# Kernel tuning notes

Hardware: AMD Instinct MI355X
Metric: run time of the kernel (lower is better)

## Reference

```python
import jax, jax.numpy as jnp
import numpy as np
import math

B = 128          # batch size
DS = 1024        # dim_s
DT = 1024        # dim_t
D = 128          # input_size (embed dim)
K = 16           # number of negatives
N = 100000       # output_size (memory bank rows)
T = 0.07         # NCE temperature
MOM = 0.5        # memory momentum


def _linear(x, W, b):
    # torch nn.Linear: y = x @ W.T + b, W is [out, in]
    return jnp.matmul(x, W.T) + b


def _l2norm(x, axis):
    # Normalize(power=2): x / (sum x^2)^(1/2)
    return x / jnp.sqrt(jnp.sum(x * x, axis=axis, keepdims=True))


def setup_inputs() -> dict:
    key = jax.random.key(0)
    ks = jax.random.split(key, 24)

    def lin_params(k1, k2, din, dout, scale=0.02):
        W = jax.random.normal(k1, (dout, din), dtype=jnp.float32) * scale
        b = jax.random.normal(k2, (dout,), dtype=jnp.float32) * scale
        return W, b

    inp = {}
    inp['s'] = jax.random.normal(ks[0], (B, DS), dtype=jnp.float32)
    inp['t'] = jax.random.normal(ks[1], (B, DT), dtype=jnp.float32)
    inp['y'] = jax.random.randint(ks[2], (B,), 0, N)
    inp['idx'] = jax.random.randint(ks[3], (B, B, K + 1), 0, N)

    stdv = 1.0 / math.sqrt(D / 3.0)
    inp['memory_s'] = jax.random.uniform(ks[4], (N, D), dtype=jnp.float32, minval=-stdv, maxval=stdv)

    inp['W_es'], inp['b_es'] = lin_params(ks[5], ks[6], DS, D)
    inp['W_et'], inp['b_et'] = lin_params(ks[7], ks[8], DT, D)
    inp['W_tv'], inp['b_tv'] = lin_params(ks[9], ks[10], D, D)
    inp['W_tq'], inp['b_tq'] = lin_params(ks[11], ks[12], D, D)
    inp['W_tsv'], inp['b_tsv'] = lin_params(ks[13], ks[14], D, D)
    inp['W_tsq'], inp['b_tsq'] = lin_params(ks[15], ks[16], D, D)
    inp['W_mt'], inp['b_mt'] = lin_params(ks[17], ks[18], D, D)
    inp['W_mts'], inp['b_mts'] = lin_params(ks[19], ks[20], D, D)
    inp['W_ht'], inp['b_ht'] = lin_params(ks[21], ks[22], D, D)
    inp['W_hts'], inp['b_hts'] = lin_params(ks[23], ks[22], D, D)
    return inp


def reference(s, t, y, idx, memory_s,
              W_es, b_es, W_et, b_et, W_tv, b_tv, W_tq, b_tq,
              W_tsv, b_tsv, W_tsq, b_tsq, W_mt, b_mt, W_mts, b_mts,
              W_ht, b_ht, W_hts, b_hts):
    idx_k = idx.reshape(B, B, -1)[:, :, :K]
    # gather negatives from memory bank (detached in the original)
    neg_s = jax.lax.stop_gradient(
        jnp.take(memory_s, idx_k.reshape(-1), axis=0).reshape(B, B, K, D))

    se = _linear(s, W_es, b_es)          # [B, D]
    te = _linear(t, W_et, b_et)          # [B, D]

    m_t_v = _linear(te, W_tv, b_tv)
    m_t_q = _linear(te, W_tq, b_tq)
    m_t_s_v = _linear(te, W_tsv, b_tsv)
    m_t_s_q_pos = _linear(se, W_tsq, b_tsq)
    m_t_s_q_neg = _linear(neg_s, W_tsq, b_tsq)   # [B, B, K, D]

    # broadcasted relation tensors: r[i, j] = relu(v[j] - q[i])
    r_t = _linear(jax.nn.relu(m_t_v[None, :, :] - m_t_q[:, None, :]), W_mt, b_mt)            # [B, B, D]
    r_t_s_pos = _linear(jax.nn.relu(m_t_s_v[None, :, :] - m_t_s_q_pos[:, None, :]), W_mts, b_mts)  # [B, B, D]
    r_t_s_neg = _linear(jax.nn.relu(m_t_s_v[None, :, None, :] - m_t_s_q_neg), W_mts, b_mts)  # [B, B, K, D]

    h_t = _l2norm(_linear(r_t, W_ht, b_ht), -1)                 # [B, B, D]
    h_t_s_pos = _l2norm(_linear(r_t_s_pos, W_hts, b_hts), -1)   # [B, B, D]
    h_t_s_neg = _l2norm(_linear(r_t_s_neg, W_hts, b_hts), -1)   # [B, B, K, D]
    h_t_s = jnp.concatenate([h_t_s_pos[:, :, None, :], h_t_s_neg], axis=2)  # [B, B, K+1, D]

    # momentum scatter update of the memory bank (no_grad in original)
    ab = jnp.take(memory_s, y, axis=0) * MOM + jax.lax.stop_gradient(se) * (1.0 - MOM)
    updated = ab / jnp.sqrt(jnp.sum(ab * ab, axis=1, keepdims=True))
    memory_new = memory_s.at[y].set(updated)

    scores = jnp.sum(h_t[:, :, None, :] * h_t_s, axis=3, keepdims=True)  # [B, B, K+1, 1]
    out = jnp.exp(scores / T) / jnp.exp(1.0 / T)
    return out.reshape(B * B, K + 1, 1), memory_new
```

## Files before the change

### kernel.cpp

```cpp
#include <hip/hip_runtime.h>


#define BB   128
#define DD   128
#define KK   16
#define NMEM 100000

static constexpr float INV_T = 1.0f / 0.07f;

#define WS_SE    0
#define WS_TE    16384
#define WS_MTV   32768
#define WS_MTQ   49152
#define WS_MSV   65536
#define WS_MSPQ  81920
#define WS_HT    98304
#define FR_TS_HI 2195456
#define FR_TS_LO 2203648
#define FR_T_HI  2211840
#define FR_T_LO  2220032
#define BC_TS    2244608
#define BC_T     2244736
#define WS_PROJ  2244864
#define OUT_MEM  278528

typedef __attribute__((ext_vector_type(8))) short short8v;
typedef __attribute__((ext_vector_type(4))) float f32x4;

__device__ inline void split2(float x0, float x1, unsigned& hi, unsigned& lo) {
    unsigned u0 = __float_as_uint(x0), u1 = __float_as_uint(x1);
    unsigned h0 = (u0 + 0x8000u) & 0xffff0000u;
    unsigned h1 = (u1 + 0x8000u) & 0xffff0000u;
    float l0 = x0 - __uint_as_float(h0);
    float l1 = x1 - __uint_as_float(h1);
    unsigned v0 = __float_as_uint(l0) + 0x8000u;
    unsigned v1 = __float_as_uint(l1) + 0x8000u;
    hi = __builtin_amdgcn_perm(h1, h0, 0x07060302u);
    lo = __builtin_amdgcn_perm(v1, v0, 0x07060302u);
}

__device__ inline void split8(const float4& x0, const float4& x1, short8v& h8, short8v& l8) {
    uint4 H, L;
    split2(x0.x, x0.y, H.x, L.x);
    split2(x0.z, x0.w, H.y, L.y);
    split2(x1.x, x1.y, H.z, L.z);
    split2(x1.z, x1.w, H.w, L.w);
    h8 = *(short8v*)&H;
    l8 = *(short8v*)&L;
}

__device__ inline void splits(float x, unsigned short& h, unsigned short& l) {
    unsigned u = __float_as_uint(x);
    unsigned hu = (u + 0x8000u) & 0xffff0000u;
    float lf = x - __uint_as_float(hu);
    h = (unsigned short)(hu >> 16);
    l = (unsigned short)((__float_as_uint(lf) + 0x8000u) >> 16);
}

__global__ __launch_bounds__(512, 2) void k_pre1b(
    const float* __restrict__ s, const float* __restrict__ t,
    const float* __restrict__ W_es, const float* __restrict__ b_es,
    const float* __restrict__ W_et, const float* __restrict__ b_et,
    const float* __restrict__ W_mts, const float* __restrict__ b_mts,
    const float* __restrict__ W_hts, const float* __restrict__ b_hts,
    const float* __restrict__ W_mt,  const float* __restrict__ b_mt,
    const float* __restrict__ W_ht,  const float* __restrict__ b_ht,
    float* __restrict__ ws)
{
    __shared__ float red[8][2048];
    int bid = blockIdx.x, tid = threadIdx.x;

    if (bid >= 16) {
        int cb = bid - 16;
        int which = cb >> 5;
        int sub = cb & 31;
        const float* A  = which ? W_ht : W_hts;
        const float* Bm = which ? W_mt : W_mts;
        short* FH = (short*)(ws + (which ? FR_T_HI : FR_TS_HI));
        short* FL = (short*)(ws + (which ? FR_T_LO : FR_TS_LO));

        int d = sub * 4 + (tid >> 7);
        int k = tid & 127;
        const float* Ar = A + d * 128;
        float acc = 0.f;
        #pragma unroll 8
        for (int m = 0; m < 128; ++m)
            acc = fmaf(Ar[m], Bm[m * 128 + k], acc);

        int t2 = d >> 4, col = d & 15, c = k >> 5, kg = (k >> 3) & 3, e = k & 7;
        int a2 = (((t2 * 4 + c) * 4 + kg) * 16 + col) * 8 + e;
        unsigned short h, l; splits(acc, h, l);
        FH[a2] = (short)h;
        FL[a2] = (short)l;

        if (sub == 0 && tid < 128) {
            const float* bin  = which ? b_mt : b_mts;
            const float* bout = which ? b_ht : b_hts;
            float a = bout[tid];
            #pragma unroll 8
            for (int m = 0; m < 128; ++m) a = fmaf(A[tid * 128 + m], bin[m], a);
            ws[(which ? BC_T : BC_TS) + tid] = a;
        }
        return;
    }

    int which = bid >> 3;
    int grp = bid & 7;
    const float* x    = which ? t : s;
    const float* W    = which ? W_et : W_es;
    const float* bias = which ? b_et : b_es;

    int lane = tid & 63, w = tid >> 6;
    int col = lane & 15, rq = lane >> 4;
    const float* xr = x + (long)(grp * 16 + col) * 1024;

    f32x4 acc[8];
    #pragma unroll
    for (int t2 = 0; t2 < 8; ++t2) {
        acc[t2][0] = 0.f; acc[t2][1] = 0.f; acc[t2][2] = 0.f; acc[t2][3] = 0.f;
    }

    #pragma unroll
    for (int c = 0; c < 4; ++c) {
        int kb = w * 128 + c * 32 + rq * 8;
        short8v ah, al;
        {
            float4 x0 = *(const float4*)&xr[kb];
            float4 x1 = *(const float4*)&xr[kb + 4];
            split8(x0, x1, ah, al);
        }
        #pragma unroll
        for (int t2 = 0; t2 < 8; ++t2) {
            const float* wr = W + (long)(t2 * 16 + col) * 1024 + kb;
            float4 w0 = *(const float4*)&wr[0];
            float4 w1 = *(const float4*)&wr[4];
            short8v bh, bl; split8(w0, w1, bh, bl);
            acc[t2] = __builtin_amdgcn_mfma_f32_16x16x32_bf16(al, bh, acc[t2], 0, 0, 0);
            acc[t2] = __builtin_amdgcn_mfma_f32_16x16x32_bf16(ah, bl, acc[t2], 0, 0, 0);
            acc[t2] = __builtin_amdgcn_mfma_f32_16x16x32_bf16(ah, bh, acc[t2], 0, 0, 0);
        }
    }

    #pragma unroll
    for (int t2 = 0; t2 < 8; ++t2)
        #pragma unroll
        for (int r = 0; r < 4; ++r)
            red[w][(rq * 4 + r) * 128 + t2 * 16 + col] = acc[t2][r];
    __syncthreads();

    for (int i = tid; i < 2048; i += 512) {
        float sum = 0.f;
        #pragma unroll
        for (int w2 = 0; w2 < 8; ++w2) sum += red[w2][i];
        int rl = i >> 7, d = i & 127;
        ws[(which ? WS_TE : WS_SE) + (grp * 16 + rl) * 128 + d] = sum + bias[d];
    }
}

__global__ __launch_bounds__(512, 2) void k_proj4(
    const float* __restrict__ W_tv,  const float* __restrict__ b_tv,
    const float* __restrict__ W_tq,  const float* __restrict__ b_tq,
    const float* __restrict__ W_tsv, const float* __restrict__ b_tsv,
    const float* __restrict__ W_tsq, const float* __restrict__ b_tsq,
    float* __restrict__ ws)
{
    int pb = blockIdx.x;
    int tid = threadIdx.x;
    int gi = tid >> 7, d = tid & 127;
    int rr = pb * 4 + gi;
    int which = rr >> 7, r = rr & 127;
    const float *W, *bias, *in;
    float* outp;
    switch (which) {
        case 0:  W = W_tv;  bias = b_tv;  in = ws + WS_TE; outp = ws + WS_MTV;  break;
        case 1:  W = W_tq;  bias = b_tq;  in = ws + WS_TE; outp = ws + WS_MTQ;  break;
        case 2:  W = W_tsv; bias = b_tsv; in = ws + WS_TE; outp = ws + WS_MSV;  break;
        default: W = W_tsq; bias = b_tsq; in = ws + WS_SE; outp = ws + WS_MSPQ; break;
    }
    const float* xr = in + r * DD;
    const float* Wr = W + d * DD;
    float a0 = 0.f, a1 = 0.f, a2 = 0.f, a3 = 0.f;
    #pragma unroll
    for (int k = 0; k < DD; k += 16) {
        float4 xv0 = *(const float4*)&xr[k],      wv0 = *(const float4*)&Wr[k];
        float4 xv1 = *(const float4*)&xr[k + 4],  wv1 = *(const float4*)&Wr[k + 4];
        float4 xv2 = *(const float4*)&xr[k + 8],  wv2 = *(const float4*)&Wr[k + 8];
        float4 xv3 = *(const float4*)&xr[k + 12], wv3 = *(const float4*)&Wr[k + 12];
        a0 = fmaf(xv0.x, wv0.x, fmaf(xv0.y, wv0.y, fmaf(xv0.z, wv0.z, fmaf(xv0.w, wv0.w, a0))));
        a1 = fmaf(xv1.x, wv1.x, fmaf(xv1.y, wv1.y, fmaf(xv1.z, wv1.z, fmaf(xv1.w, wv1.w, a1))));
        a2 = fmaf(xv2.x, wv2.x, fmaf(xv2.y, wv2.y, fmaf(xv2.z, wv2.z, fmaf(xv2.w, wv2.w, a2))));
        a3 = fmaf(xv3.x, wv3.x, fmaf(xv3.y, wv3.y, fmaf(xv3.z, wv3.z, fmaf(xv3.w, wv3.w, a3))));
    }
    outp[r * DD + d] = bias[d] + ((a0 + a1) + (a2 + a3));
}

__global__ __launch_bounds__(512, 2) void k_pre2c(
    const float* __restrict__ mem, const float* __restrict__ b_tsq,
    const float* __restrict__ W_tsq,
    float* __restrict__ ws, float* __restrict__ proj)
{
    __shared__ short Bh[16384], Bl[16384];
    int bid = blockIdx.x, tid = threadIdx.x;

    if (bid < 782) {
        {
            int d = tid >> 2, k0 = (tid & 3) * 32;
            int tt = d >> 4, col = d & 15;
            #pragma unroll
            for (int h = 0; h < 4; ++h) {
                int k = k0 + h * 8;
                float4 x0 = *(const float4*)&W_tsq[d * 128 + k];
                float4 x1 = *(const float4*)&W_tsq[d * 128 + k + 4];
                short8v h8, l8; split8(x0, x1, h8, l8);
                int c = k >> 5, kg = (k >> 3) & 3;
                int a2 = (((tt * 4 + c) * 4 + kg) * 16 + col) * 8;
                *(short8v*)&Bh[a2] = h8;
                *(short8v*)&Bl[a2] = l8;
            }
        }
        __syncthreads();

        int lane = tid & 63, w = tid >> 6;
        int g = bid * 8 + w;
        if (g >= 6250) return;

        int col = lane & 15, rq = lane >> 4;
        long rowA = (long)g * 16 + col;
        int kg = rq * 8;
        const float* src = mem + rowA * 128;

        short8v ah[4], al[4];
        #pragma unroll
        for (int c = 0; c < 4; ++c) {
            int ko = c * 32 + kg;
            float4 x0 = *(const float4*)&src[ko];
            float4 x1 = *(const float4*)&src[ko + 4];
            split8(x0, x1, ah[c], al[c]);
        }

        #pragma unroll
        for (int t = 0; t < 8; ++t) {
            float b0 = b_tsq[t * 16 + col];
            f32x4 a; a[0] = b0; a[1] = b0; a[2] = b0; a[3] = b0;
            #pragma unroll
            for (int c = 0; c < 4; ++c) {
                int off = ((t * 4 + c) * 64 + lane) * 8;
                short8v bh = *(const short8v*)&Bh[off];
                short8v bl = *(const short8v*)&Bl[off];
                a = __builtin_amdgcn_mfma_f32_16x16x32_bf16(al[c], bh, a, 0, 0, 0);
                a = __builtin_amdgcn_mfma_f32_16x16x32_bf16(ah[c], bl, a, 0, 0, 0);
                a = __builtin_amdgcn_mfma_f32_16x16x32_bf16(ah[c], bh, a, 0, 0, 0);
            }
            #pragma unroll
            for (int r = 0; r < 4; ++r)
                proj[((long)g * 16 + rq * 4 + r) * 128 + t * 16 + col] = a[r];
        }
        return;
    }

    {
        const short* frh = (const short*)(ws + FR_T_HI);
        const short* frl = (const short*)(ws + FR_T_LO);
        for (int i2 = tid; i2 < 2048; i2 += 512) {
            ((uint4*)Bh)[i2] = ((const uint4*)frh)[i2];
            ((uint4*)Bl)[i2] = ((const uint4*)frl)[i2];
        }
        __syncthreads();

        const float* mtv = ws + WS_MTV;
        const float* mtq = ws + WS_MTQ;
        const float* bc  = ws + BC_T;
        float* ht = ws + WS_HT;

        int lane = tid & 63, w = tid >> 6;
        int col = lane & 15, rq = lane >> 4;
        int g = (bid - 782) * 8 + w;
        int p = g * 16 + col;
        int i = p >> 7, j = p & 127;
        int kg = rq * 8;
        const float* vj = mtv + j * 128;
        const float* qi = mtq + i * 128;

        short8v ah[4], al[4];
        #pragma unroll
        for (int c = 0; c < 4; ++c) {
            int ko = c * 32 + kg;
            float4 v0 = *(const float4*)&vj[ko], v1 = *(const float4*)&vj[ko + 4];
            float4 q0 = *(const float4*)&qi[ko], q1 = *(const float4*)&qi[ko + 4];
            float4 r0 = make_float4(fmaxf(v0.x - q0.x, 0.f), fmaxf(v0.y - q0.y, 0.f),
                                    fmaxf(v0.z - q0.z, 0.f), fmaxf(v0.w - q0.w, 0.f));
            float4 r1 = make_float4(fmaxf(v1.x - q1.x, 0.f), fmaxf(v1.y - q1.y, 0.f),
                                    fmaxf(v1.z - q1.z, 0.f), fmaxf(v1.w - q1.w, 0.f));
            split8(r0, r1, ah[c], al[c]);
        }

        f32x4 acc[8];
        #pragma unroll
        for (int t = 0; t < 8; ++t) {
            float b0 = bc[t * 16 + col];
            f32x4 a; a[0] = b0; a[1] = b0; a[2] = b0; a[3] = b0;
            #pragma unroll
            for (int c = 0; c < 4; ++c) {
                int off = ((t * 4 + c) * 64 + lane) * 8;
                short8v bh = *(const short8v*)&Bh[off];
                short8v bl = *(const short8v*)&Bl[off];
                a = __builtin_amdgcn_mfma_f32_16x16x32_bf16(al[c], bh, a, 0, 0, 0);
                a = __builtin_amdgcn_mfma_f32_16x16x32_bf16(ah[c], bl, a, 0, 0, 0);
                a = __builtin_amdgcn_mfma_f32_16x16x32_bf16(ah[c], bh, a, 0, 0, 0);
            }
            acc[t] = a;
        }

        #pragma unroll
        for (int r = 0; r < 4; ++r) {
            long rho = g * 16 + rq * 4 + r;
            float s_uu = 0.f;
            #pragma unroll
            for (int t = 0; t < 8; ++t) { float u = acc[t][r]; s_uu = fmaf(u, u, s_uu); }
            #pragma unroll
            for (int m = 1; m < 16; m <<= 1) s_uu += __shfl_xor(s_uu, m);
            float rn = rsqrtf(s_uu);
            #pragma unroll
            for (int t = 0; t < 8; ++t)
                ht[rho * 128 + t * 16 + col] = acc[t][r] * rn;
        }
    }
}

__global__ __launch_bounds__(1024, 8) void k_neg_mfma(
    const float* __restrict__ ws, const int* __restrict__ idx,
    const float* __restrict__ proj, float* __restrict__ out,
    const float* __restrict__ mem, float* __restrict__ dst)
{
    int tid = threadIdx.x;
    if (blockIdx.x >= 1088) {
        long n4 = (long)NMEM * 128 / 4;
        long i = (long)(blockIdx.x - 1088) * 1024 + tid;
        for (; i < n4; i += 128 * 1024)
            ((float4*)dst)[i] = ((const float4*)mem)[i];
        return;
    }

    __shared__ short Bh[16384], Bl[16384];
    const short* frh = (const short*)(ws + FR_TS_HI);
    const short* frl = (const short*)(ws + FR_TS_LO);
    for (int i2 = tid; i2 < 2048; i2 += 1024) {
        ((uint4*)Bh)[i2] = ((const uint4*)frh)[i2];
        ((uint4*)Bl)[i2] = ((const uint4*)frl)[i2];
    }
    __syncthreads();

    const float* msv  = ws + WS_MSV;
    const float* mspq = ws + WS_MSPQ;
    const float* ht   = ws + WS_HT;
    const float* bc   = ws + BC_TS;

    int lane = tid & 63, w = tid >> 6;
    int col = lane & 15, rq = lane >> 4;
    int bswz = (blockIdx.x & 7) * 136 + (blockIdx.x >> 3);
    int g = bswz * 16 + w;

    int rowA = g * 16 + col;
    int p = rowA / 17;
    int slot = rowA - p * 17;
    const float* src = slot ? (proj + (long)idx[p * 17 + slot - 1] * 128)
                            : (mspq + (p >> 7) * 128);
    const float* vj = msv + (p & 127) * 128;
    int kg = rq * 8;

    short8v ah[4], al[4];
    #pragma unroll
    for (int c = 0; c < 4; ++c) {
        int ko = c * 32 + kg;
        float4 v0 = *(const float4*)&vj[ko],  v1 = *(const float4*)&vj[ko + 4];
        float4 q0 = *(const float4*)&src[ko], q1 = *(const float4*)&src[ko + 4];
        float4 r0 = make_float4(fmaxf(v0.x - q0.x, 0.f), fmaxf(v0.y - q0.y, 0.f),
                                fmaxf(v0.z - q0.z, 0.f), fmaxf(v0.w - q0.w, 0.f));
        float4 r1 = make_float4(fmaxf(v1.x - q1.x, 0.f), fmaxf(v1.y - q1.y, 0.f),
                                fmaxf(v1.z - q1.z, 0.f), fmaxf(v1.w - q1.w, 0.f));
        split8(r0, r1, ah[c], al[c]);
    }

    f32x4 acc[8];
    #pragma unroll
    for (int t = 0; t < 8; ++t) {
        float b0 = bc[t * 16 + col];
        f32x4 a; a[0] = b0; a[1] = b0; a[2] = b0; a[3] = b0;
        #pragma unroll
        for (int c = 0; c < 4; ++c) {
            int off = ((t * 4 + c) * 64 + lane) * 8;
            short8v bh = *(const short8v*)&Bh[off];
            short8v bl = *(const short8v*)&Bl[off];
            a = __builtin_amdgcn_mfma_f32_16x16x32_bf16(al[c], bh, a, 0, 0, 0);
            a = __builtin_amdgcn_mfma_f32_16x16x32_bf16(ah[c], bl, a, 0, 0, 0);
            a = __builtin_amdgcn_mfma_f32_16x16x32_bf16(ah[c], bh, a, 0, 0, 0);
        }
        acc[t] = a;
    }

    #pragma unroll
    for (int r = 0; r < 4; ++r) {
        int rho = g * 16 + rq * 4 + r;
        int pe = rho / 17;
        const float* hrow = ht + (long)pe * 128 + col;
        float s_uu = 0.f, s_hu = 0.f;
        #pragma unroll
        for (int t = 0; t < 8; ++t) {
            float u = acc[t][r];
            s_uu = fmaf(u, u, s_uu);
            s_hu = fmaf(hrow[t * 16], u, s_hu);
        }
        #pragma unroll
        for (int m = 1; m < 16; m <<= 1) {
            s_uu += __shfl_xor(s_uu, m);
            s_hu += __shfl_xor(s_hu, m);
        }
        if (col == 0)
            out[rho] = __expf((s_hu * rsqrtf(s_uu) - 1.0f) * INV_T);
    }
}

__global__ __launch_bounds__(128) void k_memupd(
    const float* __restrict__ mem, const float* __restrict__ se,
    const int* __restrict__ y, float* __restrict__ dst)
{
    int b = blockIdx.x;
    int d = threadIdx.x;
    int yb = y[b];
    for (int b2 = b + 1; b2 < BB; ++b2)
        if (y[b2] == yb) return;

    float ab = 0.5f * mem[(long)yb * 128 + d] + 0.5f * se[b * 128 + d];
    float ss = ab * ab;
    #pragma unroll
    for (int mq = 32; mq; mq >>= 1) ss += __shfl_xor(ss, mq);
    __shared__ float partial[2];
    if ((d & 63) == 0) partial[d >> 6] = ss;
    __syncthreads();
    float tot = partial[0] + partial[1];
    dst[(long)yb * 128 + d] = ab * rsqrtf(tot);
}

extern "C" void kernel_launch(void* const* d_in, const int* in_sizes, int n_in,
                              void* d_out, int out_size, void* d_ws, size_t ws_size,
                              hipStream_t stream)
{
    const float* s     = (const float*)d_in[0];
    const float* t     = (const float*)d_in[1];
    const int*   y     = (const int*)  d_in[2];
    const int*   idx   = (const int*)  d_in[3];
    const float* mem   = (const float*)d_in[4];
    const float* W_es  = (const float*)d_in[5];  const float* b_es  = (const float*)d_in[6];
    const float* W_et  = (const float*)d_in[7];  const float* b_et  = (const float*)d_in[8];
    const float* W_tv  = (const float*)d_in[9];  const float* b_tv  = (const float*)d_in[10];
    const float* W_tq  = (const float*)d_in[11]; const float* b_tq  = (const float*)d_in[12];
    const float* W_tsv = (const float*)d_in[13]; const float* b_tsv = (const float*)d_in[14];
    const float* W_tsq = (const float*)d_in[15]; const float* b_tsq = (const float*)d_in[16];
    const float* W_mt  = (const float*)d_in[17]; const float* b_mt  = (const float*)d_in[18];
    const float* W_mts = (const float*)d_in[19]; const float* b_mts = (const float*)d_in[20];
    const float* W_ht  = (const float*)d_in[21]; const float* b_ht  = (const float*)d_in[22];
    const float* W_hts = (const float*)d_in[23]; const float* b_hts = (const float*)d_in[24];

    float* out  = (float*)d_out;
    float* ws   = (float*)d_ws;
    float* proj = ws + WS_PROJ;

    k_pre1b   <<<80, 512, 0, stream>>>(s, t, W_es, b_es, W_et, b_et,
                                       W_mts, b_mts, W_hts, b_hts,
                                       W_mt, b_mt, W_ht, b_ht, ws);
    k_proj4   <<<128, 512, 0, stream>>>(W_tv, b_tv, W_tq, b_tq, W_tsv, b_tsv,
                                        W_tsq, b_tsq, ws);
    k_pre2c   <<<910, 512, 0, stream>>>(mem, b_tsq, W_tsq, ws, proj);
    k_neg_mfma<<<1216, 1024, 0, stream>>>(ws, idx, proj, out, mem, out + OUT_MEM);
    k_memupd  <<<128, 128, 0, stream>>>(mem, ws + WS_SE, y, out + OUT_MEM);
}
```

Before: 118.8 us.

## Move memory-bank projection into first kernel to overlap with encoder GEMMs

The memory-bank projection (mem @ W_tsq, 782 blocks) is moved out of the later pre2c kernel and into the first kernel, alongside the encoder linears and the weight-fold blocks. The h_t computation becomes its own small kernel. The bank projection depends only on inputs, so it can run concurrently with the small, latency-bound encoder work instead of queuing behind k_proj4. In exchange, the first kernel carries a uniform 64KB of shared memory for every block, and the small h_t kernel now runs alone after k_proj4.

```diff
diff --git a/kernel.cpp b/kernel.cpp
--- a/kernel.cpp
+++ b/kernel.cpp
@@ -57,7 +57,9 @@
     l = (unsigned short)((__float_as_uint(lf) + 0x8000u) >> 16);
 }
 
-__global__ __launch_bounds__(512, 2) void k_pre1b(
+__global__ __launch_bounds__(512, 2) void k_stage1(
+    const float* __restrict__ mem, const float* __restrict__ b_tsq,
+    const float* __restrict__ W_tsq,
     const float* __restrict__ s, const float* __restrict__ t,
     const float* __restrict__ W_es, const float* __restrict__ b_es,
     const float* __restrict__ W_et, const float* __restrict__ b_et,
@@ -65,13 +67,128 @@
     const float* __restrict__ W_hts, const float* __restrict__ b_hts,
     const float* __restrict__ W_mt,  const float* __restrict__ b_mt,
     const float* __restrict__ W_ht,  const float* __restrict__ b_ht,
-    float* __restrict__ ws)
-{
-    __shared__ float red[8][2048];
+    float* __restrict__ ws, float* __restrict__ proj)
+{
+    __shared__ __align__(16) char smem[65536];
+    short* Bh = (short*)smem;
+    short* Bl = (short*)(smem + 32768);
     int bid = blockIdx.x, tid = threadIdx.x;
 
-    if (bid >= 16) {
-        int cb = bid - 16;
+    if (bid < 782) {
+        {
+            int d = tid >> 2, k0 = (tid & 3) * 32;
+            int tt = d >> 4, col = d & 15;
+            #pragma unroll
+            for (int h = 0; h < 4; ++h) {
+                int k = k0 + h * 8;
+                float4 x0 = *(const float4*)&W_tsq[d * 128 + k];
+                float4 x1 = *(const float4*)&W_tsq[d * 128 + k + 4];
+                short8v h8, l8; split8(x0, x1, h8, l8);
+                int c = k >> 5, kg = (k >> 3) & 3;
+                int a2 = (((tt * 4 + c) * 4 + kg) * 16 + col) * 8;
+                *(short8v*)&Bh[a2] = h8;
+                *(short8v*)&Bl[a2] = l8;
+            }
+        }
+        __syncthreads();
+
+        int lane = tid & 63, w = tid >> 6;
+        int g = bid * 8 + w;
+        if (g >= 6250) return;
+
+        int col = lane & 15, rq = lane >> 4;
+        long rowA = (long)g * 16 + col;
+        int kg = rq * 8;
+        const float* src = mem + rowA * 128;
+
+        short8v ah[4], al[4];
+        #pragma unroll
+        for (int c = 0; c < 4; ++c) {
+            int ko = c * 32 + kg;
+            float4 x0 = *(const float4*)&src[ko];
+            float4 x1 = *(const float4*)&src[ko + 4];
+            split8(x0, x1, ah[c], al[c]);
+        }
+
+        #pragma unroll
+        for (int t2 = 0; t2 < 8; ++t2) {
+            float b0 = b_tsq[t2 * 16 + col];
+            f32x4 a; a[0] = b0; a[1] = b0; a[2] = b0; a[3] = b0;
+            #pragma unroll
+            for (int c = 0; c < 4; ++c) {
+                int off = ((t2 * 4 + c) * 64 + lane) * 8;
+                short8v bh = *(const short8v*)&Bh[off];
+                short8v bl = *(const short8v*)&Bl[off];
+                a = __builtin_amdgcn_mfma_f32_16x16x32_bf16(al[c], bh, a, 0, 0, 0);
+                a = __builtin_amdgcn_mfma_f32_16x16x32_bf16(ah[c], bl, a, 0, 0, 0);
+                a = __builtin_amdgcn_mfma_f32_16x16x32_bf16(ah[c], bh, a, 0, 0, 0);
+            }
+            #pragma unroll
+            for (int r = 0; r < 4; ++r)
+                proj[((long)g * 16 + rq * 4 + r) * 128 + t2 * 16 + col] = a[r];
+        }
+        return;
+    }
+
+    if (bid < 798) {
+        float (*red)[2048] = (float(*)[2048])smem;
+        int eb = bid - 782;
+        int which = eb >> 3;
+        int grp = eb & 7;
+        const float* x    = which ? t : s;
+        const float* W    = which ? W_et : W_es;
+        const float* bias = which ? b_et : b_es;
+
+        int lane = tid & 63, w = tid >> 6;
+        int col = lane & 15, rq = lane >> 4;
+        const float* xr = x + (long)(grp * 16 + col) * 1024;
+
+        f32x4 acc[8];
+        #pragma unroll
+        for (int t2 = 0; t2 < 8; ++t2) {
+            acc[t2][0] = 0.f; acc[t2][1] = 0.f; acc[t2][2] = 0.f; acc[t2][3] = 0.f;
+        }
+
+        #pragma unroll
+        for (int c = 0; c < 4; ++c) {
+            int kb = w * 128 + c * 32 + rq * 8;
+            short8v ah, al;
+            {
+                float4 x0 = *(const float4*)&xr[kb];
+                float4 x1 = *(const float4*)&xr[kb + 4];
+                split8(x0, x1, ah, al);
+            }
+            #pragma unroll
+            for (int t2 = 0; t2 < 8; ++t2) {
+                const float* wr = W + (long)(t2 * 16 + col) * 1024 + kb;
+                float4 w0 = *(const float4*)&wr[0];
+                float4 w1 = *(const float4*)&wr[4];
+                short8v bh, bl; split8(w0, w1, bh, bl);
+                acc[t2] = __builtin_amdgcn_mfma_f32_16x16x32_bf16(al, bh, acc[t2], 0, 0, 0);
+                acc[t2] = __builtin_amdgcn_mfma_f32_16x16x32_bf16(ah, bl, acc[t2], 0, 0, 0);
+                acc[t2] = __builtin_amdgcn_mfma_f32_16x16x32_bf16(ah, bh, acc[t2], 0, 0, 0);
+            }
+        }
+
+        #pragma unroll
+        for (int t2 = 0; t2 < 8; ++t2)
+            #pragma unroll
+            for (int r = 0; r < 4; ++r)
+                red[w][(rq * 4 + r) * 128 + t2 * 16 + col] = acc[t2][r];
+        __syncthreads();
+
+        for (int i = tid; i < 2048; i += 512) {
+            float sum = 0.f;
+            #pragma unroll
+            for (int w2 = 0; w2 < 8; ++w2) sum += red[w2][i];
+            int rl = i >> 7, d = i & 127;
+            ws[(which ? WS_TE : WS_SE) + (grp * 16 + rl) * 128 + d] = sum + bias[d];
+        }
+        return;
+    }
+
+    {
+        int cb = bid - 798;
         int which = cb >> 5;
         int sub = cb & 31;
         const float* A  = which ? W_ht : W_hts;
@@ -101,59 +218,6 @@
             for (int m = 0; m < 128; ++m) a = fmaf(A[tid * 128 + m], bin[m], a);
             ws[(which ? BC_T : BC_TS) + tid] = a;
         }
-        return;
-    }
-
-    int which = bid >> 3;
-    int grp = bid & 7;
-    const float* x    = which ? t : s;
-    const float* W    = which ? W_et : W_es;
-    const float* bias = which ? b_et : b_es;
-
-    int lane = tid & 63, w = tid >> 6;
-    int col = lane & 15, rq = lane >> 4;
-    const float* xr = x + (long)(grp * 16 + col) * 1024;
-
-    f32x4 acc[8];
-    #pragma unroll
-    for (int t2 = 0; t2 < 8; ++t2) {
-        acc[t2][0] = 0.f; acc[t2][1] = 0.f; acc[t2][2] = 0.f; acc[t2][3] = 0.f;
-    }
-
-    #pragma unroll
-    for (int c = 0; c < 4; ++c) {
-        int kb = w * 128 + c * 32 + rq * 8;
-        short8v ah, al;
-        {
-            float4 x0 = *(const float4*)&xr[kb];
-            float4 x1 = *(const float4*)&xr[kb + 4];
-            split8(x0, x1, ah, al);
-        }
-        #pragma unroll
-        for (int t2 = 0; t2 < 8; ++t2) {
-            const float* wr = W + (long)(t2 * 16 + col) * 1024 + kb;
-            float4 w0 = *(const float4*)&wr[0];
-            float4 w1 = *(const float4*)&wr[4];
-            short8v bh, bl; split8(w0, w1, bh, bl);
-            acc[t2] = __builtin_amdgcn_mfma_f32_16x16x32_bf16(al, bh, acc[t2], 0, 0, 0);
-            acc[t2] = __builtin_amdgcn_mfma_f32_16x16x32_bf16(ah, bl, acc[t2], 0, 0, 0);
-            acc[t2] = __builtin_amdgcn_mfma_f32_16x16x32_bf16(ah, bh, acc[t2], 0, 0, 0);
-        }
-    }
-
-    #pragma unroll
-    for (int t2 = 0; t2 < 8; ++t2)
-        #pragma unroll
-        for (int r = 0; r < 4; ++r)
-            red[w][(rq * 4 + r) * 128 + t2 * 16 + col] = acc[t2][r];
-    __syncthreads();
-
-    for (int i = tid; i < 2048; i += 512) {
-        float sum = 0.f;
-        #pragma unroll
-        for (int w2 = 0; w2 < 8; ++w2) sum += red[w2][i];
-        int rl = i >> 7, d = i & 127;
-        ws[(which ? WS_TE : WS_SE) + (grp * 16 + rl) * 128 + d] = sum + bias[d];
     }
 }
 
@@ -194,136 +258,74 @@
     outp[r * DD + d] = bias[d] + ((a0 + a1) + (a2 + a3));
 }
 
-__global__ __launch_bounds__(512, 2) void k_pre2c(
-    const float* __restrict__ mem, const float* __restrict__ b_tsq,
-    const float* __restrict__ W_tsq,
-    float* __restrict__ ws, float* __restrict__ proj)
+__global__ __launch_bounds__(512, 2) void k_ht(float* __restrict__ ws)
 {
     __shared__ short Bh[16384], Bl[16384];
-    int bid = blockIdx.x, tid = threadIdx.x;
-
-    if (bid < 782) {
-        {
-            int d = tid >> 2, k0 = (tid & 3) * 32;
-            int tt = d >> 4, col = d & 15;
-            #pragma unroll
-            for (int h = 0; h < 4; ++h) {
-                int k = k0 + h * 8;
-                float4 x0 = *(const float4*)&W_tsq[d * 128 + k];
-                float4 x1 = *(const float4*)&W_tsq[d * 128 + k + 4];
-                short8v h8, l8; split8(x0, x1, h8, l8);
-                int c = k >> 5, kg = (k >> 3) & 3;
-                int a2 = (((tt * 4 + c) * 4 + kg) * 16 + col) * 8;
-                *(short8v*)&Bh[a2] = h8;
-                *(short8v*)&Bl[a2] = l8;
-            }
-        }
-        __syncthreads();
-
-        int lane = tid & 63, w = tid >> 6;
-        int g = bid * 8 + w;
-        if (g >= 6250) return;
-
-        int col = lane & 15, rq = lane >> 4;
-        long rowA = (long)g * 16 + col;
-        int kg = rq * 8;
-        const float* src = mem + rowA * 128;
-
-        short8v ah[4], al[4];
+    const short* frh = (const short*)(ws + FR_T_HI);
+    const short* frl = (const short*)(ws + FR_T_LO);
+    int tid = threadIdx.x;
+    for (int i2 = tid; i2 < 2048; i2 += 512) {
+        ((uint4*)Bh)[i2] = ((const uint4*)frh)[i2];
+        ((uint4*)Bl)[i2] = ((const uint4*)frl)[i2];
+    }
+    __syncthreads();
+
+    const float* mtv = ws + WS_MTV;
+    const float* mtq = ws + WS_MTQ;
+    const float* bc  = ws + BC_T;
+    float* ht = ws + WS_HT;
+
+    int lane = tid & 63, w = tid >> 6;
+    int col = lane & 15, rq = lane >> 4;
+    int g = blockIdx.x * 8 + w;
+    int p = g * 16 + col;
+    int i = p >> 7, j = p & 127;
+    int kg = rq * 8;
+    const float* vj = mtv + j * 128;
+    const float* qi = mtq + i * 128;
+
+    short8v ah[4], al[4];
+    #pragma unroll
+    for (int c = 0; c < 4; ++c) {
+        int ko = c * 32 + kg;
+        float4 v0 = *(const float4*)&vj[ko], v1 = *(const float4*)&vj[ko + 4];
+        float4 q0 = *(const float4*)&qi[ko], q1 = *(const float4*)&qi[ko + 4];
+        float4 r0 = make_float4(fmaxf(v0.x - q0.x, 0.f), fmaxf(v0.y - q0.y, 0.f),
+                                fmaxf(v0.z - q0.z, 0.f), fmaxf(v0.w - q0.w, 0.f));
+        float4 r1 = make_float4(fmaxf(v1.x - q1.x, 0.f), fmaxf(v1.y - q1.y, 0.f),
+                                fmaxf(v1.z - q1.z, 0.f), fmaxf(v1.w - q1.w, 0.f));
+        split8(r0, r1, ah[c], al[c]);
+    }
+
+    f32x4 acc[8];
+    #pragma unroll
+    for (int t = 0; t < 8; ++t) {
+        float b0 = bc[t * 16 + col];
+        f32x4 a; a[0] = b0; a[1] = b0; a[2] = b0; a[3] = b0;
         #pragma unroll
         for (int c = 0; c < 4; ++c) {
-            int ko = c * 32 + kg;
-            float4 x0 = *(const float4*)&src[ko];
-            float4 x1 = *(const float4*)&src[ko + 4];
-            split8(x0, x1, ah[c], al[c]);
-        }
-
-        #pragma unroll
-        for (int t = 0; t < 8; ++t) {
-            float b0 = b_tsq[t * 16 + col];
-            f32x4 a; a[0] = b0; a[1] = b0; a[2] = b0; a[3] = b0;
-            #pragma unroll
-            for (int c = 0; c < 4; ++c) {
-                int off = ((t * 4 + c) * 64 + lane) * 8;
-                short8v bh = *(const short8v*)&Bh[off];
-                short8v bl = *(const short8v*)&Bl[off];
-                a = __builtin_amdgcn_mfma_f32_16x16x32_bf16(al[c], bh, a, 0, 0, 0);
-                a = __builtin_amdgcn_mfma_f32_16x16x32_bf16(ah[c], bl, a, 0, 0, 0);
-                a = __builtin_amdgcn_mfma_f32_16x16x32_bf16(ah[c], bh, a, 0, 0, 0);
-            }
-            #pragma unroll
-            for (int r = 0; r < 4; ++r)
-                proj[((long)g * 16 + rq * 4 + r) * 128 + t * 16 + col] = a[r];
-        }
-        return;
-    }
-
-    {
-        const short* frh = (const short*)(ws + FR_T_HI);
-        const short* frl = (const short*)(ws + FR_T_LO);
-        for (int i2 = tid; i2 < 2048; i2 += 512) {
-            ((uint4*)Bh)[i2] = ((const uint4*)frh)[i2];
-            ((uint4*)Bl)[i2] = ((const uint4*)frl)[i2];
-        }
-        __syncthreads();
-
-        const float* mtv = ws + WS_MTV;
-        const float* mtq = ws + WS_MTQ;
-        const float* bc  = ws + BC_T;
-        float* ht = ws + WS_HT;
-
-        int lane = tid & 63, w = tid >> 6;
-        int col = lane & 15, rq = lane >> 4;
-        int g = (bid - 782) * 8 + w;
-        int p = g * 16 + col;
-        int i = p >> 7, j = p & 127;
-        int kg = rq * 8;
-        const float* vj = mtv + j * 128;
-        const float* qi = mtq + i * 128;
-
-        short8v ah[4], al[4];
-        #pragma unroll
-        for (int c = 0; c < 4; ++c) {
-            int ko = c * 32 + kg;
-            float4 v0 = *(const float4*)&vj[ko], v1 = *(const float4*)&vj[ko + 4];
-            float4 q0 = *(const float4*)&qi[ko], q1 = *(const float4*)&qi[ko + 4];
-            float4 r0 = make_float4(fmaxf(v0.x - q0.x, 0.f), fmaxf(v0.y - q0.y, 0.f),
-                                    fmaxf(v0.z - q0.z, 0.f), fmaxf(v0.w - q0.w, 0.f));
-            float4 r1 = make_float4(fmaxf(v1.x - q1.x, 0.f), fmaxf(v1.y - q1.y, 0.f),
-                                    fmaxf(v1.z - q1.z, 0.f), fmaxf(v1.w - q1.w, 0.f));
-            split8(r0, r1, ah[c], al[c]);
-        }
-
-        f32x4 acc[8];
-        #pragma unroll
-        for (int t = 0; t < 8; ++t) {
-            float b0 = bc[t * 16 + col];
-            f32x4 a; a[0] = b0; a[1] = b0; a[2] = b0; a[3] = b0;
-            #pragma unroll
-            for (int c = 0; c < 4; ++c) {
-                int off = ((t * 4 + c) * 64 + lane) * 8;
-                short8v bh = *(const short8v*)&Bh[off];
-                short8v bl = *(const short8v*)&Bl[off];
-                a = __builtin_amdgcn_mfma_f32_16x16x32_bf16(al[c], bh, a, 0, 0, 0);
-                a = __builtin_amdgcn_mfma_f32_16x16x32_bf16(ah[c], bl, a, 0, 0, 0);
-                a = __builtin_amdgcn_mfma_f32_16x16x32_bf16(ah[c], bh, a, 0, 0, 0);
-            }
-            acc[t] = a;
-        }
-
-        #pragma unroll
-        for (int r = 0; r < 4; ++r) {
-            long rho = g * 16 + rq * 4 + r;
-            float s_uu = 0.f;
-            #pragma unroll
-            for (int t = 0; t < 8; ++t) { float u = acc[t][r]; s_uu = fmaf(u, u, s_uu); }
-            #pragma unroll
-            for (int m = 1; m < 16; m <<= 1) s_uu += __shfl_xor(s_uu, m);
-            float rn = rsqrtf(s_uu);
-            #pragma unroll
-            for (int t = 0; t < 8; ++t)
-                ht[rho * 128 + t * 16 + col] = acc[t][r] * rn;
-        }
+            int off = ((t * 4 + c) * 64 + lane) * 8;
+            short8v bh = *(const short8v*)&Bh[off];
+            short8v bl = *(const short8v*)&Bl[off];
+            a = __builtin_amdgcn_mfma_f32_16x16x32_bf16(al[c], bh, a, 0, 0, 0);
+            a = __builtin_amdgcn_mfma_f32_16x16x32_bf16(ah[c], bl, a, 0, 0, 0);
+            a = __builtin_amdgcn_mfma_f32_16x16x32_bf16(ah[c], bh, a, 0, 0, 0);
+        }
+        acc[t] = a;
+    }
+
+    #pragma unroll
+    for (int r = 0; r < 4; ++r) {
+        long rho = g * 16 + rq * 4 + r;
+        float s_uu = 0.f;
+        #pragma unroll
+        for (int t = 0; t < 8; ++t) { float u = acc[t][r]; s_uu = fmaf(u, u, s_uu); }
+        #pragma unroll
+        for (int m = 1; m < 16; m <<= 1) s_uu += __shfl_xor(s_uu, m);
+        float rn = rsqrtf(s_uu);
+        #pragma unroll
+        for (int t = 0; t < 8; ++t)
+            ht[rho * 128 + t * 16 + col] = acc[t][r] * rn;
     }
 }
 
@@ -465,12 +467,13 @@
     float* ws   = (float*)d_ws;
     float* proj = ws + WS_PROJ;
 
-    k_pre1b   <<<80, 512, 0, stream>>>(s, t, W_es, b_es, W_et, b_et,
-                                       W_mts, b_mts, W_hts, b_hts,
-                                       W_mt, b_mt, W_ht, b_ht, ws);
+    k_stage1  <<<862, 512, 0, stream>>>(mem, b_tsq, W_tsq,
+                                        s, t, W_es, b_es, W_et, b_et,
+                                        W_mts, b_mts, W_hts, b_hts,
+                                        W_mt, b_mt, W_ht, b_ht, ws, proj);
     k_proj4   <<<128, 512, 0, stream>>>(W_tv, b_tv, W_tq, b_tq, W_tsv, b_tsv,
                                         W_tsq, b_tsq, ws);
-    k_pre2c   <<<910, 512, 0, stream>>>(mem, b_tsq, W_tsq, ws, proj);
+    k_ht      <<<128, 512, 0, stream>>>(ws);
     k_neg_mfma<<<1216, 1024, 0, stream>>>(ws, idx, proj, out, mem, out + OUT_MEM);
     k_memupd  <<<128, 128, 0, stream>>>(mem, ws + WS_SE, y, out + OUT_MEM);
 }
```

New measurement: 119.2 us. No clear change (+0.4%).
